# Performance work log

Measured on AMD Instinct MI355X. Metric: run time of the kernel, lower is better.

The kernel has to match this reference:

```python
import jax, jax.numpy as jnp
import numpy as np
import math

BZ, SEQ, NV, VA, HA = 16, 5, 1, 8, 8
C, DSTATE, DCONV, EXPAND, NLAYER = 384, 16, 4, 2, 4
DI = EXPAND * C
DTR = math.ceil(C / 16)  # 24
NTOK = (NV + 2) * SEQ * VA * HA  # 960 multi-modal tokens
T = NTOK + 2                     # + 2 gps tokens


def _ln(x, g, b, eps=1e-5):
    m = jnp.mean(x, -1, keepdims=True)
    v = jnp.mean((x - m) ** 2, -1, keepdims=True)
    return (x - m) * jax.lax.rsqrt(v + eps) * g + b


def _mamba(x, in_w, cw, cb, xw, dtw, dtb, a_log, d, ow):
    # x: (B,T,C); Mamba with bias=False in/out proj, conv_bias=True (mamba_ssm defaults)
    xz = jnp.einsum('btc,ec->bte', x, in_w)            # (B,T,2*DI)
    xh, z = jnp.split(xz, 2, axis=-1)
    xt = jnp.swapaxes(xh, 1, 2)                        # (B,DI,T)
    xt = jax.lax.conv_general_dilated(
        xt, cw[:, None, :], (1,), [(DCONV - 1, 0)],
        feature_group_count=DI, dimension_numbers=('NCH', 'OIH', 'NCH'))
    xh = jax.nn.silu(jnp.swapaxes(xt, 1, 2) + cb)      # causal depthwise conv + SiLU
    xdbl = jnp.einsum('btd,ed->bte', xh, xw)           # (B,T,DTR+2*DS)
    dt, Bm, Cm = jnp.split(xdbl, [DTR, DTR + DSTATE], axis=-1)
    dt = jax.nn.softplus(jnp.einsum('btr,dr->btd', dt, dtw) + dtb)  # (B,T,DI)
    A = -jnp.exp(a_log)                                # (DI,DSTATE)

    def step(h, inp):
        dt_t, x_t, b_t, c_t = inp                      # (B,DI),(B,DI),(B,DS),(B,DS)
        h = h * jnp.exp(dt_t[..., None] * A) + (dt_t * x_t)[..., None] * b_t[:, None, :]
        return h, jnp.einsum('bds,bs->bd', h, c_t)

    h0 = jnp.zeros((x.shape[0], DI, DSTATE), x.dtype)
    xs = tuple(jnp.swapaxes(a, 0, 1) for a in (dt, xh, Bm, Cm))
    _, ys = jax.lax.scan(step, h0, xs)
    y = jnp.swapaxes(ys, 0, 1) + d * xh
    y = y * jax.nn.silu(z)
    return jnp.einsum('btd,cd->btc', y, ow)


def _forward(image_tensor, lidar_tensor, radar_tensor, gps, pos_emb,
             ln1_g, ln1_b, fc1_w, fc1_b, fc2_w, fc2_b,
             in_proj_w, conv_w, conv_b, x_proj_w, dt_proj_w, dt_proj_b,
             A_log, D_param, out_proj_w, ln_f_g, ln_f_b):
    bz = lidar_tensor.shape[0] // SEQ
    h, w = lidar_tensor.shape[2], lidar_tensor.shape[3]
    img = image_tensor.reshape(bz, NV * SEQ, -1, h, w)
    lid = lidar_tensor.reshape(bz, SEQ, -1, h, w)
    rad = radar_tensor.reshape(bz, SEQ, -1, h, w)
    s1, s2 = C // 3, C // 3 * 2
    cs_img = jnp.concatenate([img[:, :, :s1], lid[:, :, s1:s2], rad[:, :, s2:]], axis=2)
    cs_lid = jnp.concatenate([lid[:, :, :s1], rad[:, :, s1:s2], img[:, :, s2:]], axis=2)
    cs_rad = jnp.concatenate([rad[:, :, :s1], img[:, :, s1:s2], lid[:, :, s2:]], axis=2)
    tok = jnp.concatenate([cs_img, cs_lid, cs_rad], axis=1)     # (bz, 3*SEQ, C, h, w)
    tok = jnp.transpose(tok, (0, 1, 3, 4, 2)).reshape(bz, -1, C)
    tok = jnp.concatenate([tok, gps], axis=1)                   # (bz, T, C)
    x = pos_emb + tok                                           # dropout is identity (eval)
    for l in range(NLAYER):
        x_ln = _ln(x, ln1_g[l], ln1_b[l])
        x_fc1 = jnp.einsum('btc,ec->bte', x_ln, fc1_w[l]) + fc1_b[l]
        x_fm = _mamba(x_fc1, in_proj_w[l, 0], conv_w[l, 0], conv_b[l, 0],
                      x_proj_w[l, 0], dt_proj_w[l, 0], dt_proj_b[l, 0],
                      A_log[l, 0], D_param[l, 0], out_proj_w[l, 0])
        x_flip = jnp.flip(x_fc1, axis=1)
        x_bm = _mamba(x_flip, in_proj_w[l, 1], conv_w[l, 1], conv_b[l, 1],
                      x_proj_w[l, 1], dt_proj_w[l, 1], dt_proj_b[l, 1],
                      A_log[l, 1], D_param[l, 1], out_proj_w[l, 1])
        x_fc2 = jnp.einsum('btc,ec->bte', x_flip, fc2_w[l]) + fc2_b[l]
        x_relu = jnp.where(x_fc2 >= 0, x_fc2, 0.2 * x_fc2)      # LeakyReLU(0.2)
        x = x_bm * x_relu + x_fm * x_bm                         # note: x_bm stays flipped, as in original
    x = _ln(x, ln_f_g, ln_f_b)
    pos_out = x[:, NTOK:]
    x = x[:, :NTOK].reshape(bz, (NV + 2) * SEQ, VA, HA, C)
    x = jnp.transpose(x, (0, 1, 4, 2, 3))
    img_out = x[:, :NV * SEQ].reshape(bz * NV * SEQ, -1, h, w)
    lid_out = x[:, NV * SEQ:(NV + 1) * SEQ].reshape(bz * SEQ, -1, h, w)
    rad_out = x[:, (NV + 1) * SEQ:].reshape(bz * SEQ, -1, h, w)
    return img_out, lid_out, rad_out, pos_out


def setup_inputs() -> dict:
    key = jax.random.key(0)
    it = iter(jax.random.split(key, 24))

    def n(shape, s=0.02):
        return jax.random.normal(next(it), shape, jnp.float32) * s

    return dict(
        image_tensor=n((BZ * NV * SEQ, C, VA, HA), 1.0),
        lidar_tensor=n((BZ * SEQ, C, VA, HA), 1.0),
        radar_tensor=n((BZ * SEQ, C, VA, HA), 1.0),
        gps=n((BZ, 2, C), 1.0),
        pos_emb=n((1, T, C), 0.02),
        ln1_g=jnp.ones((NLAYER, C)), ln1_b=jnp.zeros((NLAYER, C)),
        fc1_w=n((NLAYER, C, C)), fc1_b=jnp.zeros((NLAYER, C)),
        fc2_w=n((NLAYER, C, C)), fc2_b=jnp.zeros((NLAYER, C)),
        in_proj_w=n((NLAYER, 2, 2 * DI, C)),
        conv_w=n((NLAYER, 2, DI, DCONV), 0.1),
        conv_b=jnp.zeros((NLAYER, 2, DI)),
        x_proj_w=n((NLAYER, 2, DTR + 2 * DSTATE, DI)),
        dt_proj_w=n((NLAYER, 2, DI, DTR), 0.1),
        dt_proj_b=jnp.full((NLAYER, 2, DI), -4.6, jnp.float32),  # softplus ~ 0.01
        A_log=jnp.tile(jnp.log(jnp.arange(1., DSTATE + 1, dtype=jnp.float32)), (NLAYER, 2, DI, 1)),
        D_param=jnp.ones((NLAYER, 2, DI)),
        out_proj_w=n((NLAYER, 2, C, DI)),
        ln_f_g=jnp.ones((C,)), ln_f_b=jnp.zeros((C,)),
    )


def reference(image_tensor, lidar_tensor, radar_tensor, gps, pos_emb,
              ln1_g, ln1_b, fc1_w, fc1_b, fc2_w, fc2_b,
              in_proj_w, conv_w, conv_b, x_proj_w, dt_proj_w, dt_proj_b,
              A_log, D_param, out_proj_w, ln_f_g, ln_f_b):
    return _forward(image_tensor, lidar_tensor, radar_tensor, gps, pos_emb,
                    ln1_g, ln1_b, fc1_w, fc1_b, fc2_w, fc2_b,
                    in_proj_w, conv_w, conv_b, x_proj_w, dt_proj_w, dt_proj_b,
                    A_log, D_param, out_proj_w, ln_f_g, ln_f_b)
```

## Files before the change

kernel.cpp:

```cpp
#include <hip/hip_runtime.h>
#include <cstdint>
#include <cstddef>


constexpr int BZv = 16, SEQ = 5, NV = 1;
constexpr int C = 384, DSTATE = 16, DCONV = 4, NLAYER = 4;
constexpr int DI = 768;
constexpr int DTR = 24;
constexpr int NTOK = (NV + 2) * SEQ * 64;
constexpr int T = NTOK + 2;
constexpr int M = BZv * T;
constexpr int HB = 8;
constexpr int MH = HB * T;
constexpr int XZdim = 2 * DI;
constexpr int ND = DTR + 2 * DSTATE;
constexpr int NCHUNK = 37, TC = 26;
constexpr int NQ8 = 121;
constexpr size_t SEC_SZ = (size_t)BZv * SEQ * C * 64;

constexpr size_t SET1 = (size_t)C * C;
constexpr size_t SETI = (size_t)2 * DI * C;
constexpr size_t SETO = (size_t)C * DI;
constexpr size_t SETX = (size_t)64 * DI;
constexpr size_t WSZ1 = 4 * SET1;
constexpr size_t WSZI = 8 * SETI;
constexpr size_t WSZO = 8 * SETO;
constexpr size_t WSZX = 8 * SETX;

typedef __attribute__((ext_vector_type(8))) short short8;
typedef __attribute__((ext_vector_type(4))) float floatx4;

#define GLOAD_LDS16(g, l)                                        \
  __builtin_amdgcn_global_load_lds(                              \
      (const __attribute__((address_space(1))) void*)(g),        \
      (__attribute__((address_space(3))) void*)(l), 16, 0, 0)

__device__ __forceinline__ void split_bf16(float v, short& hi, short& lo) {
  unsigned u = __float_as_uint(v);
  unsigned hib = u & 0xFFFF0000u;
  float r = v - __uint_as_float(hib);
  hi = (short)(hib >> 16);
  lo = (short)(__float_as_uint(r) >> 16);
}

__device__ __forceinline__ float join_bf16(short h, short l) {
  return __uint_as_float((unsigned)(unsigned short)h << 16) +
         __uint_as_float((unsigned)(unsigned short)l << 16);
}

__device__ __forceinline__ void pow16(float e1, float* e) {
  e[0] = e1;
  e[1] = e1 * e1;
  e[3] = e[1] * e[1];
  e[7] = e[3] * e[3];
  e[15] = e[7] * e[7];
  e[2] = e[1] * e[0];
  e[4] = e[3] * e[0];
  e[5] = e[3] * e[1];
  e[6] = e[5] * e[0];
  e[8] = e[7] * e[0];
  e[9] = e[7] * e[1];
  e[10] = e[9] * e[0];
  e[11] = e[7] * e[3];
  e[12] = e[11] * e[0];
  e[13] = e[11] * e[1];
  e[14] = e[13] * e[0];
}

__global__ __launch_bounds__(256) void assemble_t_k(
    const float* __restrict__ img, const float* __restrict__ lid,
    const float* __restrict__ rad, const float* __restrict__ gps,
    const float* __restrict__ pe, float* __restrict__ x) {
  __shared__ float lds[64][129];
  int blk = blockIdx.x, tid = threadIdx.x;
  if (blk < 720) {
    int b = blk / 45;
    int rem = blk % 45;
    int g_ = rem / 3, cc = rem % 3;
    int sec = g_ / 5, s = g_ % 5;
    int srow = b * 5 + s;
    int which = (cc + sec) % 3;
    const float* src = (which == 0) ? img : (which == 1 ? lid : rad);
    const float* sp = src + (size_t)srow * (C * 64) + cc * 8192;
#pragma unroll
    for (int i = 0; i < 32; i++) {
      int lin = tid + 256 * i;
      lds[lin & 63][lin >> 6] = sp[lin];
    }
    __syncthreads();
#pragma unroll
    for (int i = 0; i < 32; i++) {
      int lin = tid + 256 * i;
      int p = lin >> 7, c = lin & 127;
      int t = g_ * 64 + p;
      int ccc = cc * 128 + c;
      x[((size_t)b * T + t) * C + ccc] = lds[p][c] + pe[(size_t)t * C + ccc];
    }
  } else {
#pragma unroll
    for (int i = 0; i < 48; i++) {
      int lin = tid + 256 * i;
      int r = lin / C, c = lin % C;
      int b = r >> 1, e = r & 1;
      x[((size_t)b * T + NTOK + e) * C + c] =
          gps[((size_t)b * 2 + e) * C + c] + pe[(size_t)(NTOK + e) * C + c];
    }
  }
}

__global__ __launch_bounds__(256) void ln_fused_k(
    const float* __restrict__ x, const float* __restrict__ g,
    const float* __restrict__ b, short* __restrict__ oh,
    short* __restrict__ ol) {
  int row = blockIdx.x * 4 + (threadIdx.x >> 6);
  int lane = threadIdx.x & 63;
  const float* xr = x + (size_t)row * C;
  float v[6];
  float s = 0.f;
#pragma unroll
  for (int j = 0; j < 6; j++) {
    v[j] = xr[lane + 64 * j];
    s += v[j];
  }
#pragma unroll
  for (int o = 32; o > 0; o >>= 1) s += __shfl_xor(s, o, 64);
  float mean = s * (1.f / 384.f);
  float q = 0.f;
#pragma unroll
  for (int j = 0; j < 6; j++) {
    float d = v[j] - mean;
    q += d * d;
  }
#pragma unroll
  for (int o = 32; o > 0; o >>= 1) q += __shfl_xor(q, o, 64);
  float rstd = rsqrtf(q * (1.f / 384.f) + 1e-5f);
#pragma unroll
  for (int j = 0; j < 6; j++) {
    int c = lane + 64 * j;
    float val = (v[j] - mean) * rstd * g[c] + b[c];
    short h, l;
    split_bf16(val, h, l);
    oh[(size_t)row * C + c] = h;
    ol[(size_t)row * C + c] = l;
  }
}

__global__ __launch_bounds__(256) void ln_stats2_k(const float* __restrict__ x,
                                                   float* __restrict__ stats) {
  int row = blockIdx.x * 4 + (threadIdx.x >> 6);
  int lane = threadIdx.x & 63;
  const float* xr = x + (size_t)row * C;
  float v[6];
  float s = 0.f;
#pragma unroll
  for (int j = 0; j < 6; j++) {
    v[j] = xr[lane + 64 * j];
    s += v[j];
  }
#pragma unroll
  for (int o = 32; o > 0; o >>= 1) s += __shfl_xor(s, o, 64);
  float mean = s * (1.f / 384.f);
  float q = 0.f;
#pragma unroll
  for (int j = 0; j < 6; j++) {
    float d = v[j] - mean;
    q += d * d;
  }
#pragma unroll
  for (int o = 32; o > 0; o >>= 1) q += __shfl_xor(q, o, 64);
  if (lane == 0) {
    stats[2 * row] = mean;
    stats[2 * row + 1] = rsqrtf(q * (1.f / 384.f) + 1e-5f);
  }
}

template <int NSRC, int KSRC, int KS>
__global__ __launch_bounds__(256) void cast_swz_k(const float* __restrict__ src,
                                                  short* __restrict__ oh,
                                                  short* __restrict__ ol) {
  constexpr int NP = (NSRC + 15) & ~15;
  constexpr size_t SETSZ = (size_t)NP * KS * 32;
  int set = blockIdx.y;
  size_t idx = (size_t)blockIdx.x * 256 + threadIdx.x;
  int e = (int)(idx & 7);
  int lane = (int)((idx >> 3) & 63);
  size_t rest = idx >> 9;
  int ks = (int)(rest % KS);
  int nf = (int)(rest / KS);
  int n = nf * 16 + (lane & 15);
  int k = ks * 32 + ((lane >> 4) << 3) + e;
  float v = 0.f;
  if (n < NSRC && k < KSRC)
    v = src[(size_t)set * NSRC * KSRC + (size_t)n * KSRC + k];
  short h, l;
  split_bf16(v, h, l);
  oh[(size_t)set * SETSZ + idx] = h;
  ol[(size_t)set * SETSZ + idx] = l;
}

template <int ACT, bool BIAS, bool FLIPA, bool OSPLIT, bool SWAPXY, bool XSWZ>
__global__ __launch_bounds__(256) void mgemm_k(
    const short* __restrict__ Ah, const short* __restrict__ Al, int K,
    const short* __restrict__ Wh, const short* __restrict__ Wl, int N,
    const float* __restrict__ bias, float* __restrict__ Co, int ldc,
    short* __restrict__ Oh, short* __restrict__ Ol, int Mrows, int arow_off,
    int crow_off, int nt, int mpx) {
  __shared__ __align__(16) short sAh[128 * 32];
  __shared__ __align__(16) short sAl[128 * 32];
  const int tid = threadIdx.x;
  const int wave = tid >> 6, lane = tid & 63;
  int bm_, bn_;
  if constexpr (XSWZ) {
    const int f = blockIdx.x;
    const int xcd = f & 7, j = f >> 3;
    bn_ = j % nt;
    bm_ = xcd * mpx + j / nt;
  } else {
    bm_ = SWAPXY ? blockIdx.x : blockIdx.y;
    bn_ = SWAPXY ? blockIdx.y : blockIdx.x;
  }
  const int m0 = bm_ * 128, n0 = bn_ * 128;
  const int lrow = lane >> 2, lchunk = lane & 3;
  const int wm = (wave >> 1) * 64, wn = (wave & 1) * 64;
  const int frow = lane & 15, fquad = lane >> 4;
  const int KST = K >> 5;
  const int nfb = (n0 + wn) >> 4;

  size_t arow[2];
#pragma unroll
  for (int p = 0; p < 2; p++) {
    int r = p * 64 + wave * 16 + lrow;
    int lm = m0 + r;
    if (lm >= Mrows) lm = Mrows - 1;
    int g = arow_off + lm;
    if (FLIPA) {
      int bb = g / T;
      int tt = g - bb * T;
      g = bb * T + (T - 1 - tt);
    }
    arow[p] = (size_t)g * K;
  }

  floatx4 acc[4][4] = {};
  for (int k0 = 0; k0 < K; k0 += 32) {
    if (k0) __syncthreads();
    const int kc = k0 + lchunk * 8;
#pragma unroll
    for (int p = 0; p < 2; p++) {
      GLOAD_LDS16(Ah + arow[p] + kc, &sAh[(p * 64 + wave * 16) * 32]);
      GLOAD_LDS16(Al + arow[p] + kc, &sAl[(p * 64 + wave * 16) * 32]);
    }
    const int ks = k0 >> 5;
    short8 bh[4], bl[4];
#pragma unroll
    for (int j = 0; j < 4; j++) {
      size_t bo = (((size_t)(nfb + j) * KST + ks) * 64 + lane) * 8;
      bh[j] = *(const short8*)&Wh[bo];
      bl[j] = *(const short8*)&Wl[bo];
    }
    __syncthreads();
    short8 ah[4], al[4];
#pragma unroll
    for (int i = 0; i < 4; i++) {
      int ra = (wm + i * 16 + frow) * 32 + fquad * 8;
      ah[i] = *(const short8*)&sAh[ra];
      al[i] = *(const short8*)&sAl[ra];
    }
#pragma unroll
    for (int i = 0; i < 4; i++)
#pragma unroll
      for (int j = 0; j < 4; j++) {
        acc[i][j] = __builtin_amdgcn_mfma_f32_16x16x32_bf16(ah[i], bh[j],
                                                            acc[i][j], 0, 0, 0);
        acc[i][j] = __builtin_amdgcn_mfma_f32_16x16x32_bf16(al[i], bh[j],
                                                            acc[i][j], 0, 0, 0);
        acc[i][j] = __builtin_amdgcn_mfma_f32_16x16x32_bf16(ah[i], bl[j],
                                                            acc[i][j], 0, 0, 0);
      }
  }
#pragma unroll
  for (int i = 0; i < 4; i++) {
#pragma unroll
    for (int r = 0; r < 4; r++) {
      int gm = m0 + wm + i * 16 + fquad * 4 + r;
      if (gm >= Mrows) continue;
      int grow = crow_off + gm;
#pragma unroll
      for (int j = 0; j < 4; j++) {
        int gn = n0 + wn + j * 16 + frow;
        if (gn >= N) continue;
        float v = acc[i][j][r];
        if constexpr (BIAS) v += bias[gn];
        if constexpr (ACT == 1) v = v >= 0.f ? v : 0.2f * v;
        if constexpr (OSPLIT) {
          short h, l;
          split_bf16(v, h, l);
          Oh[(size_t)grow * N + gn] = h;
          Ol[(size_t)grow * N + gn] = l;
        } else {
          Co[(size_t)grow * ldc + gn] = v;
        }
      }
    }
  }
}

template <int ACT, bool BIAS, int MT = 64, bool XSWZ = false>
__global__ __launch_bounds__(256) void mgemm64_k(
    const short* __restrict__ Ah, const short* __restrict__ Al, int lda, int K,
    const short* __restrict__ Wh, const short* __restrict__ Wl, int N,
    const float* __restrict__ bias, float* __restrict__ Co, int ldc,
    const float* __restrict__ e1, const float* __restrict__ e2, int Mrows,
    int crow_off, int nt, int mpx) {
  __shared__ __align__(16) short sAh[MT * 32];
  __shared__ __align__(16) short sAl[MT * 32];
  const int tid = threadIdx.x;
  const int wave = tid >> 6, lane = tid & 63;
  int bm_, bn_;
  if constexpr (XSWZ) {
    const int f = blockIdx.x;
    const int xcd = f & 7, j = f >> 3;
    bn_ = j % nt;
    bm_ = xcd * mpx + j / nt;
  } else {
    bm_ = blockIdx.y;
    bn_ = blockIdx.x;
  }
  const int m0 = bm_ * MT, n0 = bn_ * 64;
  const int schunk = tid & 3;
  const int frow = lane & 15, fquad = lane >> 4;
  const int KST = K >> 5;
  const int nfw = (n0 >> 4) + wave;

  int lm = m0 + ((MT == 64) ? (tid >> 2) : (lane >> 2));
  if (lm >= Mrows) lm = Mrows - 1;
  size_t aoff = (size_t)lm * lda;

  floatx4 acc[MT / 16] = {};
  for (int k0 = 0; k0 < K; k0 += 32) {
    if (k0) __syncthreads();
    const int kc = k0 + schunk * 8;
    if constexpr (MT == 64) {
      GLOAD_LDS16(Ah + aoff + kc, &sAh[(wave * 16) * 32]);
      GLOAD_LDS16(Al + aoff + kc, &sAl[(wave * 16) * 32]);
    } else {
      if (wave == 0) GLOAD_LDS16(Ah + aoff + kc, &sAh[0]);
      if (wave == 1) GLOAD_LDS16(Al + aoff + kc, &sAl[0]);
    }
    const int ks = k0 >> 5;
    short8 bh, bl;
    {
      size_t bo = (((size_t)nfw * KST + ks) * 64 + lane) * 8;
      bh = *(const short8*)&Wh[bo];
      bl = *(const short8*)&Wl[bo];
    }
    __syncthreads();
    short8 ah[MT / 16], al[MT / 16];
#pragma unroll
    for (int i = 0; i < MT / 16; i++) {
      int ra = (i * 16 + frow) * 32 + fquad * 8;
      ah[i] = *(const short8*)&sAh[ra];
      al[i] = *(const short8*)&sAl[ra];
    }
#pragma unroll
    for (int i = 0; i < MT / 16; i++) {
      acc[i] = __builtin_amdgcn_mfma_f32_16x16x32_bf16(ah[i], bh, acc[i], 0, 0, 0);
      acc[i] = __builtin_amdgcn_mfma_f32_16x16x32_bf16(al[i], bh, acc[i], 0, 0, 0);
      acc[i] = __builtin_amdgcn_mfma_f32_16x16x32_bf16(ah[i], bl, acc[i], 0, 0, 0);
    }
  }
  const int gn = n0 + wave * 16 + frow;
  if (gn < N) {
#pragma unroll
    for (int i = 0; i < MT / 16; i++) {
#pragma unroll
      for (int r = 0; r < 4; r++) {
        int gm = m0 + i * 16 + fquad * 4 + r;
        if (gm >= Mrows) continue;
        int grow = crow_off + gm;
        float v = acc[i][r];
        if constexpr (BIAS) v += bias[gn];
        if constexpr (ACT == 4) {
          size_t o = (size_t)grow * ldc + gn;
          v = e2[o] * (e1[o] + v);
        }
        Co[(size_t)grow * ldc + gn] = v;
      }
    }
  }
}

__global__ __launch_bounds__(256) void conv_k(const float* __restrict__ xz,
                                              const float* __restrict__ cw,
                                              const float* __restrict__ cb,
                                              short* __restrict__ xch,
                                              short* __restrict__ xcl) {
  int idx = blockIdx.x * 256 + threadIdx.x;
  int dh = idx % (DI / 2);
  int rem = idx / (DI / 2);
  int q = rem % NQ8;
  int b = rem / NQ8;
  int d = dh * 2;
  int t0 = q * 8;
  const float* base = xz + (size_t)b * T * XZdim + d;
  float4 cwa = *(const float4*)&cw[d * 4];
  float4 cwb = *(const float4*)&cw[(d + 1) * 4];
  float cb0 = cb[d], cb1 = cb[d + 1];
  float2 w[11];
#pragma unroll
  for (int j = 0; j < 11; j++) {
    int tt = t0 - 3 + j;
    w[j] = (tt >= 0 && tt < T) ? *(const float2*)(base + (size_t)tt * XZdim)
                               : make_float2(0.f, 0.f);
  }
  const float cwx[4] = {cwa.x, cwa.y, cwa.z, cwa.w};
  const float cwy[4] = {cwb.x, cwb.y, cwb.z, cwb.w};
#pragma unroll
  for (int r = 0; r < 8; r++) {
    int t = t0 + r;
    if (t >= T) break;
    float a0 = cb0, a1 = cb1;
#pragma unroll
    for (int j = 0; j < 4; j++) {
      a0 += w[r + j].x * cwx[j];
      a1 += w[r + j].y * cwy[j];
    }
    float v0 = a0 / (1.f + __expf(-a0));
    float v1 = a1 / (1.f + __expf(-a1));
    short h0, l0, h1, l1;
    split_bf16(v0, h0, l0);
    split_bf16(v1, h1, l1);
    size_t o = ((size_t)b * T + t) * DI + d;
    *(short2*)&xch[o] = make_short2(h0, h1);
    *(short2*)&xcl[o] = make_short2(l0, l1);
  }
}


__global__ __launch_bounds__(256) void scan_p1_k(
    const short* __restrict__ xch, const short* __restrict__ xcl,
    const float* __restrict__ xdbc, const float* __restrict__ dtw,
    const float* __restrict__ dtb, const float* __restrict__ alog,
    float* __restrict__ hchk, float* __restrict__ sdt) {
  int tid = threadIdx.x;
  int d = blockIdx.x * 256 + tid;
  int ch = blockIdx.y, b = blockIdx.z;
  float wreg[DTR];
  {
    const float* wd = dtw + (size_t)d * DTR;
#pragma unroll
    for (int j = 0; j < DTR; j += 4) {
      float4 t4 = *(const float4*)(wd + j);
      wreg[j] = t4.x;
      wreg[j + 1] = t4.y;
      wreg[j + 2] = t4.z;
      wreg[j + 3] = t4.w;
    }
  }
  const float dbias = dtb[d];
  float A[DSTATE], h[DSTATE];
  bool powA = true;
#pragma unroll
  for (int s = 0; s < DSTATE; s++) {
    A[s] = -expf(alog[d * DSTATE + s]);
    powA = powA && (fabsf(A[s] + (float)(s + 1)) <= 1e-4f * (float)(s + 1));
    h[s] = 0.f;
  }
  const int t0 = ch * TC;
  const short* xchr = xch + ((size_t)b * T + t0) * DI;
  const short* xclr = xcl + ((size_t)b * T + t0) * DI;
  const float* bcr = xdbc + ((size_t)b * T + t0) * 64;
  float sd = 0.f;
  if (powA) {
    for (int t = 0; t < TC; t++) {
      const float* bc = bcr + (size_t)t * 64;
      float a = dbias;
#pragma unroll
      for (int j = 0; j < DTR; j++) a = fmaf(bc[j], wreg[j], a);
      float dt = (a > 20.f) ? a : __logf(1.f + __expf(a));
      float xv = join_bf16(xchr[(size_t)t * DI + d], xclr[(size_t)t * DI + d]);
      float dx = dt * xv;
      sd += dt;
      float ev[DSTATE];
      pow16(__expf(-dt), ev);
#pragma unroll
      for (int s = 0; s < DSTATE; s++) h[s] = h[s] * ev[s] + dx * bc[24 + s];
    }
  } else {
    for (int t = 0; t < TC; t++) {
      const float* bc = bcr + (size_t)t * 64;
      float a = dbias;
#pragma unroll
      for (int j = 0; j < DTR; j++) a = fmaf(bc[j], wreg[j], a);
      float dt = (a > 20.f) ? a : __logf(1.f + __expf(a));
      float xv = join_bf16(xchr[(size_t)t * DI + d], xclr[(size_t)t * DI + d]);
      float dx = dt * xv;
      sd += dt;
#pragma unroll
      for (int s = 0; s < DSTATE; s++)
        h[s] = h[s] * __expf(dt * A[s]) + dx * bc[24 + s];
    }
  }
  size_t o = ((size_t)(b * NCHUNK + ch) * DSTATE) * DI + d;
#pragma unroll
  for (int s = 0; s < DSTATE; s++) hchk[o + (size_t)s * DI] = h[s];
  sdt[(size_t)(b * NCHUNK + ch) * DI + d] = sd;
}

__global__ __launch_bounds__(256) void scan_p2_k(float* __restrict__ hchk,
                                                 const float* __restrict__ sdt,
                                                 const float* __restrict__ alog) {
  int idx = blockIdx.x * 256 + threadIdx.x;
  int d = idx % DI;
  int rem = idx / DI;
  int s = rem % DSTATE, b = rem / DSTATE;
  float A = -expf(alog[d * DSTATE + s]);
  float hin = 0.f;
#pragma unroll
  for (int ch = 0; ch < NCHUNK; ch++) {
    size_t o = ((size_t)(b * NCHUNK + ch) * DSTATE + s) * DI + d;
    float P = __expf(A * sdt[(size_t)(b * NCHUNK + ch) * DI + d]);
    float hl = hchk[o];
    hchk[o] = hin;
    hin = P * hin + hl;
  }
}

__global__ __launch_bounds__(256) void scan_p3_k(
    const float* __restrict__ xzb, const short* __restrict__ xch,
    const short* __restrict__ xcl, const float* __restrict__ xdbc,
    const float* __restrict__ dtw, const float* __restrict__ dtb,
    const float* __restrict__ alog, const float* __restrict__ Dp,
    const float* __restrict__ hchk, short* __restrict__ yh,
    short* __restrict__ yl) {
  int tid = threadIdx.x;
  int d = blockIdx.x * 256 + tid;
  int ch = blockIdx.y, b = blockIdx.z;
  float wreg[DTR];
  {
    const float* wd = dtw + (size_t)d * DTR;
#pragma unroll
    for (int j = 0; j < DTR; j += 4) {
      float4 t4 = *(const float4*)(wd + j);
      wreg[j] = t4.x;
      wreg[j + 1] = t4.y;
      wreg[j + 2] = t4.z;
      wreg[j + 3] = t4.w;
    }
  }
  const float dbias = dtb[d];
  float A[DSTATE], h[DSTATE];
  bool powA = true;
  size_t o = ((size_t)(b * NCHUNK + ch) * DSTATE) * DI + d;
#pragma unroll
  for (int s = 0; s < DSTATE; s++) {
    A[s] = -expf(alog[d * DSTATE + s]);
    powA = powA && (fabsf(A[s] + (float)(s + 1)) <= 1e-4f * (float)(s + 1));
    h[s] = hchk[o + (size_t)s * DI];
  }
  float Dd = Dp[d];
  const int t0 = ch * TC;
  const float* xzr = xzb + ((size_t)b * T + t0) * XZdim;
  const short* xchr = xch + ((size_t)b * T + t0) * DI;
  const short* xclr = xcl + ((size_t)b * T + t0) * DI;
  const float* bcr = xdbc + ((size_t)b * T + t0) * 64;
  if (powA) {
    for (int t = 0; t < TC; t++) {
      const float* bc = bcr + (size_t)t * 64;
      float a = dbias;
#pragma unroll
      for (int j = 0; j < DTR; j++) a = fmaf(bc[j], wreg[j], a);
      float dt = (a > 20.f) ? a : __logf(1.f + __expf(a));
      float xv = join_bf16(xchr[(size_t)t * DI + d], xclr[(size_t)t * DI + d]);
      float zv = xzr[(size_t)t * XZdim + DI + d];
      float dx = dt * xv;
      float accv = 0.f;
      float ev[DSTATE];
      pow16(__expf(-dt), ev);
#pragma unroll
      for (int s = 0; s < DSTATE; s++) {
        h[s] = h[s] * ev[s] + dx * bc[24 + s];
        accv += h[s] * bc[40 + s];
      }
      float y = accv + Dd * xv;
      float sz = zv / (1.f + __expf(-zv));
      float v = y * sz;
      short hh, ll;
      split_bf16(v, hh, ll);
      size_t oi = ((size_t)(b * T + t0 + t)) * DI + d;
      yh[oi] = hh;
      yl[oi] = ll;
    }
  } else {
    for (int t = 0; t < TC; t++) {
      const float* bc = bcr + (size_t)t * 64;
      float a = dbias;
#pragma unroll
      for (int j = 0; j < DTR; j++) a = fmaf(bc[j], wreg[j], a);
      float dt = (a > 20.f) ? a : __logf(1.f + __expf(a));
      float xv = join_bf16(xchr[(size_t)t * DI + d], xclr[(size_t)t * DI + d]);
      float zv = xzr[(size_t)t * XZdim + DI + d];
      float dx = dt * xv;
      float accv = 0.f;
#pragma unroll
      for (int s = 0; s < DSTATE; s++) {
        h[s] = h[s] * __expf(dt * A[s]) + dx * bc[24 + s];
        accv += h[s] * bc[40 + s];
      }
      float y = accv + Dd * xv;
      float sz = zv / (1.f + __expf(-zv));
      float v = y * sz;
      short hh, ll;
      split_bf16(v, hh, ll);
      size_t oi = ((size_t)(b * T + t0 + t)) * DI + d;
      yh[oi] = hh;
      yl[oi] = ll;
    }
  }
}

__global__ __launch_bounds__(256) void ln_scatter_k(
    const float* __restrict__ x, const float* __restrict__ stats,
    const float* __restrict__ g, const float* __restrict__ bb,
    float* __restrict__ out) {
  __shared__ float lds[64][129];
  int blk = blockIdx.x, tid = threadIdx.x;
  if (blk < 240) {
    int b = blk / 15, g_ = blk % 15;
    int sec = g_ / 5, s = g_ % 5;
    const int rbase = b * T + g_ * 64;
    for (int cc = 0; cc < 3; cc++) {
      if (cc) __syncthreads();
#pragma unroll
      for (int i = 0; i < 32; i++) {
        int lin = tid + 256 * i;
        int p = lin >> 7, c = lin & 127;
        int row = rbase + p;
        int ccc = cc * 128 + c;
        float v = x[(size_t)row * C + ccc];
        v = (v - stats[2 * row]) * stats[2 * row + 1] * g[ccc] + bb[ccc];
        lds[p][c] = v;
      }
      __syncthreads();
      size_t obase = (size_t)sec * SEC_SZ +
                     (((size_t)(b * 5 + s) * C + cc * 128) << 6);
#pragma unroll
      for (int i = 0; i < 32; i++) {
        int lin = tid + 256 * i;
        int c = lin >> 6, p = lin & 63;
        out[obase + ((size_t)c << 6) + p] = lds[p][c];
      }
    }
  } else {
#pragma unroll
    for (int i = 0; i < 48; i++) {
      int lin = tid + 256 * i;
      int r = lin / C, c = lin % C;
      int b = r >> 1, e = r & 1;
      int row = b * T + NTOK + e;
      float v = x[(size_t)row * C + c];
      v = (v - stats[2 * row]) * stats[2 * row + 1] * g[c] + bb[c];
      out[3 * SEC_SZ + ((size_t)(b * 2 + e)) * C + c] = v;
    }
  }
}

extern "C" void kernel_launch(void* const* d_in, const int* in_sizes, int n_in,
                              void* d_out, int out_size, void* d_ws,
                              size_t ws_size, hipStream_t stream) {
  const float* image = (const float*)d_in[0];
  const float* lidar = (const float*)d_in[1];
  const float* radar = (const float*)d_in[2];
  const float* gps = (const float*)d_in[3];
  const float* pe = (const float*)d_in[4];
  const float* ln1g = (const float*)d_in[5];
  const float* ln1b = (const float*)d_in[6];
  const float* fc1w = (const float*)d_in[7];
  const float* fc1b = (const float*)d_in[8];
  const float* fc2w = (const float*)d_in[9];
  const float* fc2b_ = (const float*)d_in[10];
  const float* inw = (const float*)d_in[11];
  const float* cw = (const float*)d_in[12];
  const float* cb = (const float*)d_in[13];
  const float* xw = (const float*)d_in[14];
  const float* dtw = (const float*)d_in[15];
  const float* dtb = (const float*)d_in[16];
  const float* alog = (const float*)d_in[17];
  const float* Dp = (const float*)d_in[18];
  const float* ow = (const float*)d_in[19];
  const float* lnfg = (const float*)d_in[20];
  const float* lnfb = (const float*)d_in[21];
  float* out = (float*)d_out;

  constexpr size_t MC = (size_t)M * C;
  float* ws = (float*)d_ws;
  float* x = ws;
  float* fcb = x + MC;
  float* bmfm = fcb + MC;
  float* x1f = bmfm + MC;
  float* yf = x1f + MC;
  float* xz_h = yf + MC;
  float* xcp = xz_h + (size_t)MH * XZdim;
  float* xdbc = xcp + (size_t)MH * DI;
  float* wpl = xdbc + (size_t)MH * 64;

  short* lnh = (short*)bmfm;
  short* lnl = lnh + MC;
  float* bm = bmfm;
  short* x1h = (short*)x1f;
  short* x1l = x1h + MC;
  short* yh = (short*)yf;
  short* yl = yh + (size_t)MH * DI;
  short* xch = (short*)xcp;
  short* xcl = xch + (size_t)MH * DI;

  short* wf1h = (short*)wpl;
  short* wf1l = wf1h + WSZ1;
  short* wf2h = wf1l + WSZ1;
  short* wf2l = wf2h + WSZ1;
  short* winh = wf2l + WSZ1;
  short* winl = winh + WSZI;
  short* wowh = winl + WSZI;
  short* wowl = wowh + WSZO;
  short* wxh = wowl + WSZO;
  short* wxl = wxh + WSZX;
  float* stats2 = (float*)(wxl + WSZX);
  constexpr size_t CHK_H = (size_t)HB * NCHUNK * DSTATE * DI;
  float* hchk = stats2 + 2 * (size_t)M;
  float* sdtb = hchk + CHK_H;

  cast_swz_k<C, C, 12><<<dim3((int)(SET1 / 256), 4), 256, 0, stream>>>(
      fc1w, wf1h, wf1l);
  cast_swz_k<C, C, 12><<<dim3((int)(SET1 / 256), 4), 256, 0, stream>>>(
      fc2w, wf2h, wf2l);
  cast_swz_k<2 * DI, C, 12><<<dim3((int)(SETI / 256), 8), 256, 0, stream>>>(
      inw, winh, winl);
  cast_swz_k<C, DI, 24><<<dim3((int)(SETO / 256), 8), 256, 0, stream>>>(
      ow, wowh, wowl);
  cast_swz_k<ND, DI, 24><<<dim3((int)(SETX / 256), 8), 256, 0, stream>>>(
      xw, wxh, wxl);

  assemble_t_k<<<721, 256, 0, stream>>>(image, lidar, radar, gps, pe, x);

  for (int l = 0; l < NLAYER; l++) {
    ln_fused_k<<<M / 4, 256, 0, stream>>>(x, ln1g + l * C, ln1b + l * C, lnh,
                                          lnl);
    mgemm_k<0, true, false, true, false, true><<<384, 256, 0, stream>>>(
        lnh, lnl, C, wf1h + l * SET1, wf1l + l * SET1, C, fc1b + l * C,
        nullptr, 0, x1h, x1l, M, 0, 0, 3, 16);
    mgemm_k<1, true, true, false, false, true><<<384, 256, 0, stream>>>(
        x1h, x1l, C, wf2h + l * SET1, wf2l + l * SET1, C, fc2b_ + l * C, fcb,
        C, nullptr, nullptr, M, 0, 0, 3, 16);
    for (int di = 0; di < 2; di++) {
      const int dir = 1 - di;
      size_t wo = (size_t)(l * 2 + dir);
      for (int h = 0; h < 2; h++) {
        const int roff = h * MH;
        if (dir == 0)
          mgemm_k<0, false, false, false, false, true><<<768, 256, 0, stream>>>(
              x1h, x1l, C, winh + wo * SETI, winl + wo * SETI, 2 * DI, nullptr,
              xz_h, XZdim, nullptr, nullptr, MH, roff, 0, 12, 8);
        else
          mgemm_k<0, false, true, false, false, true><<<768, 256, 0, stream>>>(
              x1h, x1l, C, winh + wo * SETI, winl + wo * SETI, 2 * DI, nullptr,
              xz_h, XZdim, nullptr, nullptr, MH, roff, 0, 12, 8);
        conv_k<<<(HB * NQ8 * (DI / 2)) / 256, 256, 0, stream>>>(
            xz_h, cw + wo * DI * DCONV, cb + wo * DI, xch, xcl);
        mgemm64_k<0, false, 16><<<dim3(1, MH / 16), 256, 0, stream>>>(
            xch, xcl, DI, DI, wxh + wo * SETX, wxl + wo * SETX, ND, nullptr,
            xdbc, 64, nullptr, nullptr, MH, 0, 0, 0);
        scan_p1_k<<<dim3(3, NCHUNK, HB), 256, 0, stream>>>(
            xch, xcl, xdbc, dtw + wo * DI * DTR, dtb + wo * DI,
            alog + wo * DI * DSTATE, hchk, sdtb);
        scan_p2_k<<<(HB * DSTATE * DI) / 256, 256, 0, stream>>>(
            hchk, sdtb, alog + wo * DI * DSTATE);
        scan_p3_k<<<dim3(3, NCHUNK, HB), 256, 0, stream>>>(
            xz_h, xch, xcl, xdbc, dtw + wo * DI * DTR, dtb + wo * DI,
            alog + wo * DI * DSTATE, Dp + wo * DI, hchk, yh, yl);
        if (dir == 1)
          mgemm64_k<0, false, 64, true><<<768, 256, 0, stream>>>(
              yh, yl, DI, DI, wowh + wo * SETO, wowl + wo * SETO, C, nullptr,
              bm, C, nullptr, nullptr, MH, roff, 6, 16);
        else
          mgemm64_k<4, false, 64, true><<<768, 256, 0, stream>>>(
              yh, yl, DI, DI, wowh + wo * SETO, wowl + wo * SETO, C, nullptr,
              x, C, fcb, bm, MH, roff, 6, 16);
      }
    }
  }
  ln_stats2_k<<<M / 4, 256, 0, stream>>>(x, stats2);
  ln_scatter_k<<<241, 256, 0, stream>>>(x, stats2, lnfg, lnfb, out);
}
```

Measured before the change: 2.904 ms.

## Halve scan chunk length and split dt/exp precompute from the state recurrence

The chunked selective scan now uses 74 chunks of 13 timesteps instead of 37 of 26, which doubles the parallel work in the chunk passes while lengthening the sequential cross-chunk pass. In the power-of-A path, the per-timestep dt projection, softplus, exp and input loads are hoisted into a fully unrolled prologue stored in register arrays, so the serial h recurrence only does the FMA chain. The 24-term dt dot product is split into four independent accumulators to shorten its dependency chain. The register arrays and full unrolling raise register pressure, and more chunks add state traffic in the combine pass.

```diff
diff --git a/kernel.cpp b/kernel.cpp
--- a/kernel.cpp
+++ b/kernel.cpp
@@ -14,7 +14,7 @@
 constexpr int MH = HB * T;
 constexpr int XZdim = 2 * DI;
 constexpr int ND = DTR + 2 * DSTATE;
-constexpr int NCHUNK = 37, TC = 26;
+constexpr int NCHUNK = 74, TC = 13;
 constexpr int NQ8 = 121;
 constexpr size_t SEC_SZ = (size_t)BZv * SEQ * C * 64;
 
@@ -65,6 +65,20 @@
   e[12] = e[11] * e[0];
   e[13] = e[11] * e[1];
   e[14] = e[13] * e[0];
+}
+
+__device__ __forceinline__ float dot24(const float* __restrict__ bc,
+                                       const float* __restrict__ w,
+                                       float bias) {
+  float a0 = bias, a1 = 0.f, a2 = 0.f, a3 = 0.f;
+#pragma unroll
+  for (int j = 0; j < 6; j++) {
+    a0 = fmaf(bc[j], w[j], a0);
+    a1 = fmaf(bc[6 + j], w[6 + j], a1);
+    a2 = fmaf(bc[12 + j], w[12 + j], a2);
+    a3 = fmaf(bc[18 + j], w[18 + j], a3);
+  }
+  return (a0 + a1) + (a2 + a3);
 }
 
 __global__ __launch_bounds__(256) void assemble_t_k(
@@ -472,26 +486,29 @@
   const float* bcr = xdbc + ((size_t)b * T + t0) * 64;
   float sd = 0.f;
   if (powA) {
+    float e1a[TC], dxa[TC];
+#pragma unroll
     for (int t = 0; t < TC; t++) {
       const float* bc = bcr + (size_t)t * 64;
-      float a = dbias;
-#pragma unroll
-      for (int j = 0; j < DTR; j++) a = fmaf(bc[j], wreg[j], a);
+      float a = dot24(bc, wreg, dbias);
       float dt = (a > 20.f) ? a : __logf(1.f + __expf(a));
+      sd += dt;
+      e1a[t] = __expf(-dt);
       float xv = join_bf16(xchr[(size_t)t * DI + d], xclr[(size_t)t * DI + d]);
-      float dx = dt * xv;
-      sd += dt;
+      dxa[t] = dt * xv;
+    }
+#pragma unroll
+    for (int t = 0; t < TC; t++) {
+      const float* bc = bcr + (size_t)t * 64;
       float ev[DSTATE];
-      pow16(__expf(-dt), ev);
-#pragma unroll
-      for (int s = 0; s < DSTATE; s++) h[s] = h[s] * ev[s] + dx * bc[24 + s];
+      pow16(e1a[t], ev);
+#pragma unroll
+      for (int s = 0; s < DSTATE; s++) h[s] = h[s] * ev[s] + dxa[t] * bc[24 + s];
     }
   } else {
     for (int t = 0; t < TC; t++) {
       const float* bc = bcr + (size_t)t * 64;
-      float a = dbias;
-#pragma unroll
-      for (int j = 0; j < DTR; j++) a = fmaf(bc[j], wreg[j], a);
+      float a = dot24(bc, wreg, dbias);
       float dt = (a > 20.f) ? a : __logf(1.f + __expf(a));
       float xv = join_bf16(xchr[(size_t)t * DI + d], xclr[(size_t)t * DI + d]);
       float dx = dt * xv;
@@ -565,24 +582,31 @@
   const short* xclr = xcl + ((size_t)b * T + t0) * DI;
   const float* bcr = xdbc + ((size_t)b * T + t0) * 64;
   if (powA) {
+    float e1a[TC], xva[TC], dta[TC], za[TC];
+#pragma unroll
     for (int t = 0; t < TC; t++) {
       const float* bc = bcr + (size_t)t * 64;
-      float a = dbias;
-#pragma unroll
-      for (int j = 0; j < DTR; j++) a = fmaf(bc[j], wreg[j], a);
+      float a = dot24(bc, wreg, dbias);
       float dt = (a > 20.f) ? a : __logf(1.f + __expf(a));
-      float xv = join_bf16(xchr[(size_t)t * DI + d], xclr[(size_t)t * DI + d]);
-      float zv = xzr[(size_t)t * XZdim + DI + d];
-      float dx = dt * xv;
+      dta[t] = dt;
+      e1a[t] = __expf(-dt);
+      xva[t] = join_bf16(xchr[(size_t)t * DI + d], xclr[(size_t)t * DI + d]);
+      za[t] = xzr[(size_t)t * XZdim + DI + d];
+    }
+#pragma unroll
+    for (int t = 0; t < TC; t++) {
+      const float* bc = bcr + (size_t)t * 64;
+      float ev[DSTATE];
+      pow16(e1a[t], ev);
+      float dx = dta[t] * xva[t];
       float accv = 0.f;
-      float ev[DSTATE];
-      pow16(__expf(-dt), ev);
 #pragma unroll
       for (int s = 0; s < DSTATE; s++) {
         h[s] = h[s] * ev[s] + dx * bc[24 + s];
         accv += h[s] * bc[40 + s];
       }
-      float y = accv + Dd * xv;
+      float y = accv + Dd * xva[t];
+      float zv = za[t];
       float sz = zv / (1.f + __expf(-zv));
       float v = y * sz;
       short hh, ll;
@@ -594,9 +618,7 @@
   } else {
     for (int t = 0; t < TC; t++) {
       const float* bc = bcr + (size_t)t * 64;
-      float a = dbias;
-#pragma unroll
-      for (int j = 0; j < DTR; j++) a = fmaf(bc[j], wreg[j], a);
+      float a = dot24(bc, wreg, dbias);
       float dt = (a > 20.f) ? a : __logf(1.f + __expf(a));
       float xv = join_bf16(xchr[(size_t)t * DI + d], xclr[(size_t)t * DI + d]);
       float zv = xzr[(size_t)t * XZdim + DI + d];
```

Result: slower. 3.331 ms (+14.7%).
